# Optimization experiments

Hardware: AMD Instinct MI355X
Metric: run time of the kernel (lower is better)

## Reference

```python
import jax, jax.numpy as jnp
import numpy as np

KH = KW = 3
STRIDE = 1
PAD = 1
K_CHUNK = 16  # chunk size along the C*kh*kw patch dim to bound the [N,F,kc,L] intermediate


def _unfold(x):
    # Mirrors torch.nn.functional.unfold: output [N, C*KH*KW, Ho*Wo], c-major then (kh, kw).
    N, C, H, W = x.shape
    Ho = (H - KH + 2 * PAD) // STRIDE + 1
    Wo = (W - KW + 2 * PAD) // STRIDE + 1
    xp = jnp.pad(x, ((0, 0), (0, 0), (PAD, PAD), (PAD, PAD)))
    pats = jnp.stack(
        [xp[:, :, i:i + STRIDE * Ho:STRIDE, j:j + STRIDE * Wo:STRIDE]
         for i in range(KH) for j in range(KW)],
        axis=2,
    )  # [N, C, KH*KW, Ho, Wo]
    return pats.reshape(N, C * KH * KW, Ho * Wo), Ho, Wo


def _chunk_dist(xc, wc):
    # xc: [N, kc, L], wc: [F, kc] -> partial L1 sums over this K-chunk: [N, F, L]
    return jnp.abs(xc[:, None, :, :] - wc[None, :, :, None]).sum(axis=2)


def _adder2d(x, W):
    # out[n, f, i, j] = -sum_k |Xcol[n, k, l] - Wcol[f, k]|  (AdderNet L1 'correlation')
    N = x.shape[0]
    F = W.shape[0]
    Xcol, Ho, Wo = _unfold(x)          # [N, K, L]
    Wcol = W.reshape(F, -1)            # [F, K]
    K = Wcol.shape[1]
    chunk = jax.checkpoint(_chunk_dist)  # remat so backward never stores [N,F,K,L] signs
    acc = jnp.zeros((N, F, Ho * Wo), x.dtype)
    for s in range(0, K, K_CHUNK):     # fixed structural loop over patch dim (K=288 -> 18 chunks)
        acc = acc + chunk(Xcol[:, s:s + K_CHUNK, :], Wcol[:, s:s + K_CHUNK])
    return -acc.reshape(N, F, Ho, Wo)


def setup_inputs() -> dict:
    key = jax.random.key(0)
    kx, kw = jax.random.split(key)
    x = jax.random.normal(kx, (16, 32, 56, 56), dtype=jnp.float32)
    # kaiming_normal_ scale on [64,32,3,3]: std = sqrt(2 / fan_in), fan_in = 32*3*3
    W = jax.random.normal(kw, (64, 32, 3, 3), dtype=jnp.float32) * np.sqrt(2.0 / (32 * 3 * 3)).astype(np.float32)
    return {"x": x, "W": W}


def reference(x, W):
    return _adder2d(x, W)
```

## Files before the change

### kernel.cpp

```cpp
#include <hip/hip_runtime.h>
#include <stdint.h>
#include <stddef.h>


#define N_   16
#define C_   32
#define H_   56
#define F_   64
#define HW_  3136
#define FPW  8
#define NFG  8
#define ROWB 224
#define WQ_ELTS (C_ * NFG * 96)

typedef int    int32x4 __attribute__((ext_vector_type(4)));
typedef float  f32x16  __attribute__((ext_vector_type(16)));
typedef float  f32x8   __attribute__((ext_vector_type(8)));

__device__ float  __buf_load_f32(int32x4 srsrc, int voffset, int soffset, int aux) __asm("llvm.amdgcn.raw.buffer.load.f32");
__device__ f32x16 __sbuf_load_v16(int32x4 srsrc, int soffset, int aux) __asm("llvm.amdgcn.s.buffer.load.v16f32");
__device__ f32x8  __sbuf_load_v8 (int32x4 srsrc, int soffset, int aux) __asm("llvm.amdgcn.s.buffer.load.v8f32");

__device__ inline int32x4 make_srd(const void* p, int bytes) {
    union { const void* p; uint32_t u[2]; } a; a.p = p;
    int32x4 r;
    r.x = (int)a.u[0];
    r.y = (int)a.u[1];
    r.z = bytes;
    r.w = 0x00020000;
    return r;
}

__global__ __launch_bounds__(64)
void prep_w(const float* __restrict__ w, float* __restrict__ wq) {
    int idx = blockIdx.x * 64 + threadIdx.x;
    if (idx >= WQ_ELTS) return;
    int slot = idx % 96;
    int cg   = idx / 96;
    int c    = cg / NFG;
    int fg   = cg % NFG;
    int fi   = slot / 9;
    int kk   = slot % 9;
    float v = 0.0f;
    if (slot < 72)
        v = w[((fg * 8 + fi) * C_ + c) * 9 + kk];
    wq[idx] = v;
}

__global__ __launch_bounds__(64)
void adder_main(const float* __restrict__ x,
                const float* __restrict__ wq,
                float* __restrict__ out) {
    const int lane = threadIdx.x;
    const int bid  = blockIdx.x;
    const int fg   = bid & (NFG - 1);
    const int bid2 = bid >> 3;
    const int row  = bid2 % H_;
    const int n    = bid2 / H_;
    const int f0   = fg * FPW;

    const int vA = (lane - 1) * 4;
    const int vB = lane * 4;

    const int nr0 = (row >= 1)      ? ROWB : 0;
    const int nr2 = (row <= H_ - 2) ? ROWB : 0;

    const float* xb = x + (size_t)n * C_ * HW_ + (ptrdiff_t)(row - 1) * H_;

    const int32x4 wsrd = make_srd(wq, WQ_ELTS * 4);
    const int wgbase = fg * 96 * 4;

    float acc[FPW];
#pragma unroll
    for (int f = 0; f < FPW; ++f) acc[f] = 0.0f;

    float xva[9], xvb[9];

    auto load_ch = [&](int c, float* v) {
        const float* b = xb + (size_t)c * HW_;
        int32x4 s0 = make_srd(b,          nr0);
        int32x4 s1 = make_srd(b + H_,     ROWB);
        int32x4 s2 = make_srd(b + 2 * H_, nr2);
        v[0] = __buf_load_f32(s0, vA, 0, 0);
        v[1] = __buf_load_f32(s0, vB, 0, 0);
        v[2] = __buf_load_f32(s0, vB, 4, 0);
        v[3] = __buf_load_f32(s1, vA, 0, 0);
        v[4] = __buf_load_f32(s1, vB, 0, 0);
        v[5] = __buf_load_f32(s1, vB, 4, 0);
        v[6] = __buf_load_f32(s2, vA, 0, 0);
        v[7] = __buf_load_f32(s2, vB, 0, 0);
        v[8] = __buf_load_f32(s2, vB, 4, 0);
    };

    auto compute = [&](int c, const float* cur) {
        const int wb = c * (NFG * 96 * 4) + wgbase;
        f32x16 w0 = __sbuf_load_v16(wsrd, wb,       0);
        f32x16 w1 = __sbuf_load_v16(wsrd, wb + 64,  0);
        f32x16 w2 = __sbuf_load_v16(wsrd, wb + 128, 0);
        f32x16 w3 = __sbuf_load_v16(wsrd, wb + 192, 0);
        f32x8  w4 = __sbuf_load_v8 (wsrd, wb + 256, 0);
#pragma unroll
        for (int f = 0; f < FPW; ++f) {
#pragma unroll
            for (int k = 0; k < 9; ++k) {
                const int i = f * 9 + k;
                const float wv = (i < 16) ? w0[i]
                               : (i < 32) ? w1[i - 16]
                               : (i < 48) ? w2[i - 32]
                               : (i < 64) ? w3[i - 48]
                               :            w4[i - 64];
                acc[f] += fabsf(cur[k] - wv);
            }
        }
    };

    load_ch(0, xva);
    for (int c = 0; c < C_; c += 2) {
        load_ch(c + 1, xvb);
        compute(c, xva);
        if (c + 2 < C_) load_ch(c + 2, xva);
        compute(c + 1, xvb);
    }

    if (lane < H_) {
#pragma unroll
        for (int f = 0; f < FPW; ++f)
            out[(size_t)(n * F_ + f0 + f) * HW_ + row * H_ + lane] = -acc[f];
    }
}

extern "C" void kernel_launch(void* const* d_in, const int* in_sizes, int n_in,
                              void* d_out, int out_size, void* d_ws, size_t ws_size,
                              hipStream_t stream) {
    const float* x = (const float*)d_in[0];
    const float* w = (const float*)d_in[1];
    float* out = (float*)d_out;
    float* wqp = (float*)d_ws;

    prep_w<<<dim3((WQ_ELTS + 63) / 64), dim3(64), 0, stream>>>(w, wqp);
    adder_main<<<dim3(N_ * H_ * NFG), dim3(64), 0, stream>>>(x, wqp, out);
}
```

Baseline: 76.65 us.

## Stage weights in LDS per block, drop prep kernel, use 4-wave blocks

Removes the separate weight-repacking kernel and its scalar buffer loads. Each 256-thread block now covers four output rows and first copies its filter group's weights into shared memory, and every channel step reads them back as vector LDS loads. This saves one kernel launch and the scalar-cache weight fetches. In exchange, weights now come from LDS into VGPRs, which costs extra VGPRs and LDS bandwidth per channel, and every block pays a staging step plus a barrier.

Measured after the change: 88.87 us. 1.16x slower.

```diff
diff --git a/kernel.cpp b/kernel.cpp
--- a/kernel.cpp
+++ b/kernel.cpp
@@ -11,15 +11,12 @@
 #define FPW  8
 #define NFG  8
 #define ROWB 224
-#define WQ_ELTS (C_ * NFG * 96)
+#define TPB  256
 
-typedef int    int32x4 __attribute__((ext_vector_type(4)));
-typedef float  f32x16  __attribute__((ext_vector_type(16)));
-typedef float  f32x8   __attribute__((ext_vector_type(8)));
+typedef int   int32x4 __attribute__((ext_vector_type(4)));
+typedef float f32x4   __attribute__((ext_vector_type(4)));
 
-__device__ float  __buf_load_f32(int32x4 srsrc, int voffset, int soffset, int aux) __asm("llvm.amdgcn.raw.buffer.load.f32");
-__device__ f32x16 __sbuf_load_v16(int32x4 srsrc, int soffset, int aux) __asm("llvm.amdgcn.s.buffer.load.v16f32");
-__device__ f32x8  __sbuf_load_v8 (int32x4 srsrc, int soffset, int aux) __asm("llvm.amdgcn.s.buffer.load.v8f32");
+__device__ float __buf_load_f32(int32x4 srsrc, int voffset, int soffset, int aux) __asm("llvm.amdgcn.raw.buffer.load.f32");
 
 __device__ inline int32x4 make_srd(const void* p, int bytes) {
     union { const void* p; uint32_t u[2]; } a; a.p = p;
@@ -31,33 +28,35 @@
     return r;
 }
 
-__global__ __launch_bounds__(64)
-void prep_w(const float* __restrict__ w, float* __restrict__ wq) {
-    int idx = blockIdx.x * 64 + threadIdx.x;
-    if (idx >= WQ_ELTS) return;
-    int slot = idx % 96;
-    int cg   = idx / 96;
-    int c    = cg / NFG;
-    int fg   = cg % NFG;
-    int fi   = slot / 9;
-    int kk   = slot % 9;
-    float v = 0.0f;
-    if (slot < 72)
-        v = w[((fg * 8 + fi) * C_ + c) * 9 + kk];
-    wq[idx] = v;
-}
+__global__ __launch_bounds__(TPB, 4)
+void adder_main(const float* __restrict__ x,
+                const float* __restrict__ w,
+                float* __restrict__ out) {
+    __shared__ f32x4 lds_w[C_ * 18];
 
-__global__ __launch_bounds__(64)
-void adder_main(const float* __restrict__ x,
-                const float* __restrict__ wq,
-                float* __restrict__ out) {
-    const int lane = threadIdx.x;
+    const int tid  = threadIdx.x;
+    const int lane = tid & 63;
+    const int wid  = tid >> 6;
     const int bid  = blockIdx.x;
     const int fg   = bid & (NFG - 1);
     const int bid2 = bid >> 3;
-    const int row  = bid2 % H_;
-    const int n    = bid2 / H_;
+    const int rg   = bid2 % 14;
+    const int n    = bid2 / 14;
     const int f0   = fg * FPW;
+
+    {
+        float* l = (float*)lds_w;
+        for (int e = tid; e < C_ * 72; e += TPB) {
+            int c  = e / 72;
+            int rr = e % 72;
+            int fi = rr / 9;
+            int kk = rr % 9;
+            l[e] = w[((f0 + fi) * C_ + c) * 9 + kk];
+        }
+    }
+    __syncthreads();
+
+    const int row = __builtin_amdgcn_readfirstlane(rg * 4 + wid);
 
     const int vA = (lane - 1) * 4;
     const int vB = lane * 4;
@@ -67,14 +66,12 @@
 
     const float* xb = x + (size_t)n * C_ * HW_ + (ptrdiff_t)(row - 1) * H_;
 
-    const int32x4 wsrd = make_srd(wq, WQ_ELTS * 4);
-    const int wgbase = fg * 96 * 4;
-
     float acc[FPW];
 #pragma unroll
     for (int f = 0; f < FPW; ++f) acc[f] = 0.0f;
 
     float xva[9], xvb[9];
+    f32x4 warr[18];
 
     auto load_ch = [&](int c, float* v) {
         const float* b = xb + (size_t)c * HW_;
@@ -93,23 +90,14 @@
     };
 
     auto compute = [&](int c, const float* cur) {
-        const int wb = c * (NFG * 96 * 4) + wgbase;
-        f32x16 w0 = __sbuf_load_v16(wsrd, wb,       0);
-        f32x16 w1 = __sbuf_load_v16(wsrd, wb + 64,  0);
-        f32x16 w2 = __sbuf_load_v16(wsrd, wb + 128, 0);
-        f32x16 w3 = __sbuf_load_v16(wsrd, wb + 192, 0);
-        f32x8  w4 = __sbuf_load_v8 (wsrd, wb + 256, 0);
+#pragma unroll
+        for (int j = 0; j < 18; ++j) warr[j] = lds_w[c * 18 + j];
 #pragma unroll
         for (int f = 0; f < FPW; ++f) {
 #pragma unroll
             for (int k = 0; k < 9; ++k) {
                 const int i = f * 9 + k;
-                const float wv = (i < 16) ? w0[i]
-                               : (i < 32) ? w1[i - 16]
-                               : (i < 48) ? w2[i - 32]
-                               : (i < 64) ? w3[i - 48]
-                               :            w4[i - 64];
-                acc[f] += fabsf(cur[k] - wv);
+                acc[f] += fabsf(cur[k] - warr[i >> 2][i & 3]);
             }
         }
     };
@@ -135,8 +123,5 @@
     const float* x = (const float*)d_in[0];
     const float* w = (const float*)d_in[1];
     float* out = (float*)d_out;
-    float* wqp = (float*)d_ws;
-
-    prep_w<<<dim3((WQ_ELTS + 63) / 64), dim3(64), 0, stream>>>(w, wqp);
-    adder_main<<<dim3(N_ * H_ * NFG), dim3(64), 0, stream>>>(x, wqp, out);
+    adder_main<<<dim3(N_ * 14 * NFG), dim3(TPB), 0, stream>>>(x, w, out);
 }
```

## Compute two output rows per wave and load weights via vector buffer loads

Applied to the files above, without the earlier changes.

Each block now produces two adjacent output rows, so every weight value is used against two input windows and the shared middle input rows are loaded once instead of twice. Weights are no longer fetched with scalar s_buffer loads; they come in as per-lane uniform vector buffer loads, in two groups of four filters. The grid is halved and launch bounds request occupancy of 4. The risks are more VGPR pressure from the doubled accumulators and the weight vectors, fewer blocks in flight, and weight traffic moving from the scalar cache to the vector memory path.

Result: slower. 120.3 us (+57.0%).

```diff
diff --git a/kernel.cpp b/kernel.cpp
--- a/kernel.cpp
+++ b/kernel.cpp
@@ -12,14 +12,13 @@
 #define NFG  8
 #define ROWB 224
 #define WQ_ELTS (C_ * NFG * 96)
+#define ROWS 2
 
-typedef int    int32x4 __attribute__((ext_vector_type(4)));
-typedef float  f32x16  __attribute__((ext_vector_type(16)));
-typedef float  f32x8   __attribute__((ext_vector_type(8)));
+typedef int   int32x4 __attribute__((ext_vector_type(4)));
+typedef float f32x4   __attribute__((ext_vector_type(4)));
 
-__device__ float  __buf_load_f32(int32x4 srsrc, int voffset, int soffset, int aux) __asm("llvm.amdgcn.raw.buffer.load.f32");
-__device__ f32x16 __sbuf_load_v16(int32x4 srsrc, int soffset, int aux) __asm("llvm.amdgcn.s.buffer.load.v16f32");
-__device__ f32x8  __sbuf_load_v8 (int32x4 srsrc, int soffset, int aux) __asm("llvm.amdgcn.s.buffer.load.v8f32");
+__device__ float __buf_load_f32(int32x4 srsrc, int voffset, int soffset, int aux) __asm("llvm.amdgcn.raw.buffer.load.f32");
+__device__ f32x4 __buf_load_v4 (int32x4 srsrc, int voffset, int soffset, int aux) __asm("llvm.amdgcn.raw.buffer.load.v4f32");
 
 __device__ inline int32x4 make_srd(const void* p, int bytes) {
     union { const void* p; uint32_t u[2]; } a; a.p = p;
@@ -47,85 +46,96 @@
     wq[idx] = v;
 }
 
-__global__ __launch_bounds__(64)
+__global__ __launch_bounds__(64, 4)
 void adder_main(const float* __restrict__ x,
                 const float* __restrict__ wq,
                 float* __restrict__ out) {
-    const int lane = threadIdx.x;
+    const int lane = threadIdx.x & 63;
     const int bid  = blockIdx.x;
     const int fg   = bid & (NFG - 1);
     const int bid2 = bid >> 3;
-    const int row  = bid2 % H_;
-    const int n    = bid2 / H_;
+    const int rp   = bid2 % (H_ / ROWS);
+    const int n    = bid2 / (H_ / ROWS);
+    const int row  = rp * ROWS;
     const int f0   = fg * FPW;
 
     const int vA = (lane - 1) * 4;
     const int vB = lane * 4;
 
     const int nr0 = (row >= 1)      ? ROWB : 0;
-    const int nr2 = (row <= H_ - 2) ? ROWB : 0;
+    const int nr3 = (row <= H_ - 3) ? ROWB : 0;
 
     const float* xb = x + (size_t)n * C_ * HW_ + (ptrdiff_t)(row - 1) * H_;
 
     const int32x4 wsrd = make_srd(wq, WQ_ELTS * 4);
-    const int wgbase = fg * 96 * 4;
+    const int wbase = fg * 96 * 4;
 
-    float acc[FPW];
+    float acc[FPW][ROWS];
 #pragma unroll
-    for (int f = 0; f < FPW; ++f) acc[f] = 0.0f;
+    for (int f = 0; f < FPW; ++f)
+#pragma unroll
+        for (int r = 0; r < ROWS; ++r) acc[f][r] = 0.0f;
 
-    float xva[9], xvb[9];
+    float xwa[4][3], xwb[4][3];
 
-    auto load_ch = [&](int c, float* v) {
+    auto load_x = [&](int c, float (*v)[3]) {
         const float* b = xb + (size_t)c * HW_;
         int32x4 s0 = make_srd(b,          nr0);
         int32x4 s1 = make_srd(b + H_,     ROWB);
-        int32x4 s2 = make_srd(b + 2 * H_, nr2);
-        v[0] = __buf_load_f32(s0, vA, 0, 0);
-        v[1] = __buf_load_f32(s0, vB, 0, 0);
-        v[2] = __buf_load_f32(s0, vB, 4, 0);
-        v[3] = __buf_load_f32(s1, vA, 0, 0);
-        v[4] = __buf_load_f32(s1, vB, 0, 0);
-        v[5] = __buf_load_f32(s1, vB, 4, 0);
-        v[6] = __buf_load_f32(s2, vA, 0, 0);
-        v[7] = __buf_load_f32(s2, vB, 0, 0);
-        v[8] = __buf_load_f32(s2, vB, 4, 0);
+        int32x4 s2 = make_srd(b + 2 * H_, ROWB);
+        int32x4 s3 = make_srd(b + 3 * H_, nr3);
+        v[0][0] = __buf_load_f32(s0, vA, 0, 0);
+        v[0][1] = __buf_load_f32(s0, vB, 0, 0);
+        v[0][2] = __buf_load_f32(s0, vB, 4, 0);
+        v[1][0] = __buf_load_f32(s1, vA, 0, 0);
+        v[1][1] = __buf_load_f32(s1, vB, 0, 0);
+        v[1][2] = __buf_load_f32(s1, vB, 4, 0);
+        v[2][0] = __buf_load_f32(s2, vA, 0, 0);
+        v[2][1] = __buf_load_f32(s2, vB, 0, 0);
+        v[2][2] = __buf_load_f32(s2, vB, 4, 0);
+        v[3][0] = __buf_load_f32(s3, vA, 0, 0);
+        v[3][1] = __buf_load_f32(s3, vB, 0, 0);
+        v[3][2] = __buf_load_f32(s3, vB, 4, 0);
     };
 
-    auto compute = [&](int c, const float* cur) {
-        const int wb = c * (NFG * 96 * 4) + wgbase;
-        f32x16 w0 = __sbuf_load_v16(wsrd, wb,       0);
-        f32x16 w1 = __sbuf_load_v16(wsrd, wb + 64,  0);
-        f32x16 w2 = __sbuf_load_v16(wsrd, wb + 128, 0);
-        f32x16 w3 = __sbuf_load_v16(wsrd, wb + 192, 0);
-        f32x8  w4 = __sbuf_load_v8 (wsrd, wb + 256, 0);
+    auto compute = [&](int c, const float (*xw)[3]) {
+        const int cb = c * (NFG * 96 * 4) + wbase;
 #pragma unroll
-        for (int f = 0; f < FPW; ++f) {
+        for (int g = 0; g < 2; ++g) {
+            f32x4 wv[9];
 #pragma unroll
-            for (int k = 0; k < 9; ++k) {
-                const int i = f * 9 + k;
-                const float wv = (i < 16) ? w0[i]
-                               : (i < 32) ? w1[i - 16]
-                               : (i < 48) ? w2[i - 32]
-                               : (i < 64) ? w3[i - 48]
-                               :            w4[i - 64];
-                acc[f] += fabsf(cur[k] - wv);
+            for (int j = 0; j < 9; ++j)
+                wv[j] = __buf_load_v4(wsrd, j * 16, cb + g * 144, 0);
+#pragma unroll
+            for (int fi = 0; fi < 4; ++fi) {
+#pragma unroll
+                for (int kh = 0; kh < 3; ++kh) {
+#pragma unroll
+                    for (int kw = 0; kw < 3; ++kw) {
+                        const int i = fi * 9 + kh * 3 + kw;
+                        const float wf = wv[i >> 2][i & 3];
+                        acc[g * 4 + fi][0] += fabsf(xw[kh][kw]     - wf);
+                        acc[g * 4 + fi][1] += fabsf(xw[kh + 1][kw] - wf);
+                    }
+                }
             }
         }
     };
 
-    load_ch(0, xva);
+    load_x(0, xwa);
     for (int c = 0; c < C_; c += 2) {
-        load_ch(c + 1, xvb);
-        compute(c, xva);
-        if (c + 2 < C_) load_ch(c + 2, xva);
-        compute(c + 1, xvb);
+        load_x(c + 1, xwb);
+        compute(c, xwa);
+        if (c + 2 < C_) load_x(c + 2, xwa);
+        compute(c + 1, xwb);
     }
 
     if (lane < H_) {
 #pragma unroll
         for (int f = 0; f < FPW; ++f)
-            out[(size_t)(n * F_ + f0 + f) * HW_ + row * H_ + lane] = -acc[f];
+#pragma unroll
+            for (int r = 0; r < ROWS; ++r)
+                out[(size_t)(n * F_ + f0 + f) * HW_ + (row + r) * H_ + lane] = -acc[f][r];
     }
 }
 
@@ -138,5 +148,5 @@
     float* wqp = (float*)d_ws;
 
     prep_w<<<dim3((WQ_ELTS + 63) / 64), dim3(64), 0, stream>>>(w, wqp);
-    adder_main<<<dim3(N_ * H_ * NFG), dim3(64), 0, stream>>>(x, wqp, out);
+    adder_main<<<dim3(N_ * (H_ / ROWS) * NFG), dim3(64), 0, stream>>>(x, wqp, out);
 }
```
